# Kernel tuning notes

Hardware: AMD Instinct MI355X
Metric: run time of the kernel (lower is better)

## Reference

```python
import jax, jax.numpy as jnp
import numpy as np

D_MODEL, N_HEADS, D_K, D_V = 1024, 16, 64, 64


def setup_inputs() -> dict:
    key = jax.random.key(0)
    ks = jax.random.split(key, 9)
    B, S = 8, 1024
    Q = jax.random.normal(ks[0], (B, S, D_MODEL), dtype=jnp.float32)
    K = jax.random.normal(ks[1], (B, S, D_MODEL), dtype=jnp.float32)
    V = jax.random.normal(ks[2], (B, S, D_MODEL), dtype=jnp.float32)
    # Xavier-uniform weights (gain=1): limit = sqrt(6/(fan_in+fan_out))
    lim = float(np.sqrt(6.0 / (D_MODEL + N_HEADS * D_K)))
    Wq = jax.random.uniform(ks[3], (D_MODEL, N_HEADS * D_K), minval=-lim, maxval=lim, dtype=jnp.float32)
    Wk = jax.random.uniform(ks[4], (D_MODEL, N_HEADS * D_K), minval=-lim, maxval=lim, dtype=jnp.float32)
    Wv = jax.random.uniform(ks[5], (D_MODEL, N_HEADS * D_V), minval=-lim, maxval=lim, dtype=jnp.float32)
    # nn.Linear default bias init: uniform(-1/sqrt(fan_in), 1/sqrt(fan_in))
    bl = float(1.0 / np.sqrt(D_MODEL))
    bq = jax.random.uniform(ks[6], (N_HEADS * D_K,), minval=-bl, maxval=bl, dtype=jnp.float32)
    bk = jax.random.uniform(ks[7], (N_HEADS * D_K,), minval=-bl, maxval=bl, dtype=jnp.float32)
    bv = jax.random.uniform(ks[8], (N_HEADS * D_V,), minval=-bl, maxval=bl, dtype=jnp.float32)
    return {"Q": Q, "K": K, "V": V, "Wq": Wq, "bq": bq, "Wk": Wk, "bk": bk, "Wv": Wv, "bv": bv}


def reference(Q, K, V, Wq, bq, Wk, bk, Wv, bv):
    B, S, _ = Q.shape
    # projections -> [B, H, S, d]
    q = (Q @ Wq + bq).reshape(B, S, N_HEADS, D_K).transpose(0, 2, 1, 3)
    k = (K @ Wk + bk).reshape(B, S, N_HEADS, D_K).transpose(0, 2, 1, 3)
    v = (V @ Wv + bv).reshape(B, S, N_HEADS, D_V).transpose(0, 2, 1, 3)
    scores = jnp.exp(jnp.einsum('bhqd,bhkd->bhqk', q, k) / jnp.sqrt(jnp.float32(D_K)))
    attn = scores / (jnp.sum(scores, axis=-1, keepdims=True) + 1e-8)
    ctx = jnp.einsum('bhqk,bhkd->bhqd', attn, v)  # [B,H,S,Dv]
    return ctx.transpose(0, 2, 1, 3).reshape(B, S, N_HEADS * D_V)
```

## Files before the change

### kernel.cpp

```cpp
#include <hip/hip_runtime.h>
#include <stdint.h>

#define DM 1024
#define HEADS 16
#define DHEAD 64
#define BATCH 8
#define SEQ 1024
#define MTOT 8192

typedef _Float16 half8 __attribute__((ext_vector_type(8)));
typedef float floatx4 __attribute__((ext_vector_type(4)));

__device__ __forceinline__ void glds16(const void* g, void* l) {
    __builtin_amdgcn_global_load_lds(
        (const __attribute__((address_space(1))) void*)g,
        (__attribute__((address_space(3))) void*)l, 16, 0, 0);
}

__global__ __launch_bounds__(256) void cvt_inputs(
        const float* __restrict__ Q, const float* __restrict__ K,
        const float* __restrict__ V,
        _Float16* __restrict__ qb, _Float16* __restrict__ kb, _Float16* __restrict__ vb) {
    const float* src = blockIdx.y == 0 ? Q : (blockIdx.y == 1 ? K : V);
    _Float16* dst    = blockIdx.y == 0 ? qb : (blockIdx.y == 1 ? kb : vb);
    size_t i = ((size_t)blockIdx.x * 256 + threadIdx.x) * 8;
    float4 a = *(const float4*)(src + i);
    float4 b = *(const float4*)(src + i + 4);
    half8 h;
    h[0] = (_Float16)a.x; h[1] = (_Float16)a.y; h[2] = (_Float16)a.z; h[3] = (_Float16)a.w;
    h[4] = (_Float16)b.x; h[5] = (_Float16)b.y; h[6] = (_Float16)b.z; h[7] = (_Float16)b.w;
    *(half8*)(dst + i) = h;
}

__global__ __launch_bounds__(256) void cvt_w(
        const float* __restrict__ Wq, const float* __restrict__ Wk,
        const float* __restrict__ Wv,
        _Float16* __restrict__ wqt, _Float16* __restrict__ wkt, _Float16* __restrict__ wvt) {
    __shared__ float t[32][33];
    int z = blockIdx.z;
    const float* W = z == 0 ? Wq : (z == 1 ? Wk : Wv);
    _Float16* Wt   = z == 0 ? wqt : (z == 1 ? wkt : wvt);
    int k0 = blockIdx.x * 32, n0 = blockIdx.y * 32;
    int tx = threadIdx.x, ty = threadIdx.y;
#pragma unroll
    for (int i = 0; i < 4; i++)
        t[ty + i * 8][tx] = W[(size_t)(k0 + ty + i * 8) * DM + n0 + tx];
    __syncthreads();
#pragma unroll
    for (int i = 0; i < 4; i++)
        Wt[(size_t)(n0 + ty + i * 8) * DM + k0 + tx] = (_Float16)t[tx][ty + i * 8];
}

__global__ __launch_bounds__(256) void proj_gemm(
        const _Float16* __restrict__ qb, const _Float16* __restrict__ kb,
        const _Float16* __restrict__ vb,
        const _Float16* __restrict__ wqt, const _Float16* __restrict__ wkt,
        const _Float16* __restrict__ wvt,
        const float* __restrict__ bq, const float* __restrict__ bk,
        const float* __restrict__ bv,
        _Float16* __restrict__ qh, _Float16* __restrict__ kh, _Float16* __restrict__ vT) {
    __shared__ _Float16 As[128 * 64];
    __shared__ _Float16 Bs[128 * 64];
    int z = blockIdx.z;
    const _Float16* A  = z == 0 ? qb : (z == 1 ? kb : vb);
    const _Float16* Bw = z == 0 ? wqt : (z == 1 ? wkt : wvt);
    const float* bias  = z == 0 ? bq : (z == 1 ? bk : bv);
    int m0 = blockIdx.x * 128, n0 = blockIdx.y * 128;
    int tid = threadIdx.x, wid = tid >> 6, lane = tid & 63;
    int l15 = lane & 15, quad = lane >> 4;
    int wm = wid >> 1, wn = wid & 1;

    floatx4 acc[4][4] = {};

    for (int kb_ = 0; kb_ < 16; kb_++) {
        __syncthreads();
        int k0 = kb_ * 64;
        int r = (wid * 4) * 8 + (lane >> 3);
        int pg = (lane & 7) ^ (lane >> 3);
#pragma unroll
        for (int ii = 0; ii < 4; ii++) {
            int issue = wid * 4 + ii;
            int rr = r + ii * 8;
            glds16(A  + (size_t)(m0 + rr) * DM + k0 + pg * 8, &As[issue * 512]);
            glds16(Bw + (size_t)(n0 + rr) * DM + k0 + pg * 8, &Bs[issue * 512]);
        }
        __syncthreads();
#pragma unroll
        for (int kc = 0; kc < 2; kc++) {
            half8 a[4], b[4];
#pragma unroll
            for (int mt = 0; mt < 4; mt++) {
                int row = wm * 64 + mt * 16 + l15;
                int pl = (kc * 4 + quad) ^ (l15 & 7);
                a[mt] = *(const half8*)&As[row * 64 + pl * 8];
            }
#pragma unroll
            for (int nt = 0; nt < 4; nt++) {
                int row = wn * 64 + nt * 16 + l15;
                int pl = (kc * 4 + quad) ^ (l15 & 7);
                b[nt] = *(const half8*)&Bs[row * 64 + pl * 8];
            }
#pragma unroll
            for (int mt = 0; mt < 4; mt++)
#pragma unroll
                for (int nt = 0; nt < 4; nt++)
                    acc[mt][nt] = __builtin_amdgcn_mfma_f32_16x16x32_f16(
                        a[mt], b[nt], acc[mt][nt], 0, 0, 0);
        }
    }

    float scale = (z == 0) ? 0.125f : 1.0f;
    _Float16* out = (z == 0) ? qh : ((z == 1) ? kh : vT);
#pragma unroll
    for (int nt = 0; nt < 4; nt++) {
        int col = n0 + wn * 64 + nt * 16 + l15;
        float bv_ = bias[col];
        int h = col >> 6, d = col & 63;
#pragma unroll
        for (int mt = 0; mt < 4; mt++) {
#pragma unroll
            for (int r2 = 0; r2 < 4; r2++) {
                int row = m0 + wm * 64 + mt * 16 + quad * 4 + r2;
                int b_ = row >> 10, s = row & 1023;
                float v = (acc[mt][nt][r2] + bv_) * scale;
                size_t off;
                if (z == 2) off = ((size_t)(b_ * HEADS + h)) * 65536 + (size_t)d * 1024 + s;
                else        off = ((size_t)(b_ * HEADS + h)) * 65536 + (size_t)s * 64 + d;
                out[off] = (_Float16)v;
            }
        }
    }
}

__global__ __launch_bounds__(256) void attn(
        const _Float16* __restrict__ qh, const _Float16* __restrict__ kh,
        const _Float16* __restrict__ vT, float* __restrict__ out) {
    __shared__ _Float16 Qs[4096];
    __shared__ _Float16 Ks[4096];
    __shared__ _Float16 Vs[4096];
    __shared__ _Float16 Ps[4096];
    int qt = blockIdx.x, h = blockIdx.y, b = blockIdx.z;
    size_t base = ((size_t)(b * HEADS + h)) * 65536;
    int tid = threadIdx.x, wid = tid >> 6, lane = tid & 63;
    int l15 = lane & 15, quad = lane >> 4;
    int rs = lane >> 3;
    int pg = (lane & 7) ^ rs;

#pragma unroll
    for (int ii = 0; ii < 2; ii++) {
        int issue = wid * 2 + ii;
        int r = issue * 8 + rs;
        glds16(qh + base + (size_t)(qt * 64 + r) * 64 + pg * 8, &Qs[issue * 512]);
    }
    __syncthreads();
    half8 qf[2];
    {
        int row = wid * 16 + l15;
#pragma unroll
        for (int kc = 0; kc < 2; kc++) {
            int pl = (kc * 4 + quad) ^ (l15 & 7);
            qf[kc] = *(const half8*)&Qs[row * 64 + pl * 8];
        }
    }

    floatx4 oacc[4] = {};
    float rden[4] = {0.f, 0.f, 0.f, 0.f};

    for (int kt = 0; kt < 16; kt++) {
        __syncthreads();
#pragma unroll
        for (int ii = 0; ii < 2; ii++) {
            int issue = wid * 2 + ii;
            int r = issue * 8 + rs;
            glds16(kh + base + (size_t)(kt * 64 + r) * 64 + pg * 8, &Ks[issue * 512]);
            glds16(vT + base + (size_t)r * 1024 + kt * 64 + pg * 8, &Vs[issue * 512]);
        }
        __syncthreads();

        floatx4 sacc[4] = {};
#pragma unroll
        for (int kc = 0; kc < 2; kc++) {
#pragma unroll
            for (int nt = 0; nt < 4; nt++) {
                int row = nt * 16 + l15;
                int pl = (kc * 4 + quad) ^ (l15 & 7);
                half8 bf = *(const half8*)&Ks[row * 64 + pl * 8];
                sacc[nt] = __builtin_amdgcn_mfma_f32_16x16x32_f16(qf[kc], bf, sacc[nt], 0, 0, 0);
            }
        }
#pragma unroll
        for (int nt = 0; nt < 4; nt++) {
            int kj = nt * 16 + l15;
            int pbase = wid * 1024 + (kj >> 3) * 128 + (kj & 7);
#pragma unroll
            for (int j = 0; j < 4; j++) {
                float p = __expf(sacc[nt][j]);
                rden[j] += p;
                Ps[pbase + (quad * 4 + j) * 8] = (_Float16)p;
            }
        }
#pragma unroll
        for (int kc = 0; kc < 2; kc++) {
            half8 af = *(const half8*)&Ps[wid * 1024 + (kc * 4 + quad) * 128 + l15 * 8];
#pragma unroll
            for (int nt = 0; nt < 4; nt++) {
                int row = nt * 16 + l15;
                int pl = (kc * 4 + quad) ^ (l15 & 7);
                half8 bf = *(const half8*)&Vs[row * 64 + pl * 8];
                oacc[nt] = __builtin_amdgcn_mfma_f32_16x16x32_f16(af, bf, oacc[nt], 0, 0, 0);
            }
        }
    }

#pragma unroll
    for (int j = 0; j < 4; j++) {
        float d = rden[j];
        d += __shfl_xor(d, 1, 64);
        d += __shfl_xor(d, 2, 64);
        d += __shfl_xor(d, 4, 64);
        d += __shfl_xor(d, 8, 64);
        rden[j] = 1.0f / (d + 1e-8f);
    }
#pragma unroll
    for (int nt = 0; nt < 4; nt++) {
        int col = h * 64 + nt * 16 + l15;
#pragma unroll
        for (int j = 0; j < 4; j++) {
            int s = qt * 64 + wid * 16 + quad * 4 + j;
            out[((size_t)(b * SEQ + s)) * 1024 + col] = oacc[nt][j] * rden[j];
        }
    }
}

extern "C" void kernel_launch(void* const* d_in, const int* in_sizes, int n_in,
                              void* d_out, int out_size, void* d_ws, size_t ws_size,
                              hipStream_t stream) {
    const float* Q  = (const float*)d_in[0];
    const float* K  = (const float*)d_in[1];
    const float* V  = (const float*)d_in[2];
    const float* Wq = (const float*)d_in[3];
    const float* bq = (const float*)d_in[4];
    const float* Wk = (const float*)d_in[5];
    const float* bk = (const float*)d_in[6];
    const float* Wv = (const float*)d_in[7];
    const float* bv = (const float*)d_in[8];
    float* out = (float*)d_out;

    char* ws = (char*)d_ws;
    const size_t TEN = (size_t)MTOT * DM * sizeof(_Float16);
    _Float16* qb  = (_Float16*)(ws);
    _Float16* kb  = (_Float16*)(ws + TEN);
    _Float16* vb  = (_Float16*)(ws + 2 * TEN);
    _Float16* qh  = (_Float16*)(ws + 3 * TEN);
    _Float16* kh  = (_Float16*)(ws + 4 * TEN);
    _Float16* vT  = (_Float16*)(ws + 5 * TEN);
    const size_t WTN = (size_t)DM * DM * sizeof(_Float16);
    _Float16* wqt = (_Float16*)(ws + 6 * TEN);
    _Float16* wkt = (_Float16*)(ws + 6 * TEN + WTN);
    _Float16* wvt = (_Float16*)(ws + 6 * TEN + 2 * WTN);

    cvt_inputs<<<dim3(4096, 3), 256, 0, stream>>>(Q, K, V, qb, kb, vb);
    cvt_w<<<dim3(32, 32, 3), dim3(32, 8), 0, stream>>>(Wq, Wk, Wv, wqt, wkt, wvt);
    proj_gemm<<<dim3(64, 8, 3), 256, 0, stream>>>(qb, kb, vb, wqt, wkt, wvt,
                                                  bq, bk, bv, qh, kh, vT);
    attn<<<dim3(16, 16, 8), 256, 0, stream>>>(qh, kh, vT, out);
}
```

Baseline: 302.3 us.

## Enlarge attention query tile and vectorize projection epilogue stores via swapped MFMA operands

```diff
diff --git a/kernel.cpp b/kernel.cpp
--- a/kernel.cpp
+++ b/kernel.cpp
@@ -3,12 +3,12 @@
 
 #define DM 1024
 #define HEADS 16
-#define DHEAD 64
 #define BATCH 8
 #define SEQ 1024
 #define MTOT 8192
 
 typedef _Float16 half8 __attribute__((ext_vector_type(8)));
+typedef _Float16 half4 __attribute__((ext_vector_type(4)));
 typedef float floatx4 __attribute__((ext_vector_type(4)));
 
 __device__ __forceinline__ void glds16(const void* g, void* l) {
@@ -69,6 +69,7 @@
     int tid = threadIdx.x, wid = tid >> 6, lane = tid & 63;
     int l15 = lane & 15, quad = lane >> 4;
     int wm = wid >> 1, wn = wid & 1;
+    bool swapped = (z < 2);
 
     floatx4 acc[4][4] = {};
 
@@ -100,33 +101,60 @@
                 int pl = (kc * 4 + quad) ^ (l15 & 7);
                 b[nt] = *(const half8*)&Bs[row * 64 + pl * 8];
             }
-#pragma unroll
-            for (int mt = 0; mt < 4; mt++)
-#pragma unroll
-                for (int nt = 0; nt < 4; nt++)
-                    acc[mt][nt] = __builtin_amdgcn_mfma_f32_16x16x32_f16(
-                        a[mt], b[nt], acc[mt][nt], 0, 0, 0);
-        }
-    }
-
-    float scale = (z == 0) ? 0.125f : 1.0f;
-    _Float16* out = (z == 0) ? qh : ((z == 1) ? kh : vT);
-#pragma unroll
-    for (int nt = 0; nt < 4; nt++) {
-        int col = n0 + wn * 64 + nt * 16 + l15;
-        float bv_ = bias[col];
-        int h = col >> 6, d = col & 63;
-#pragma unroll
-        for (int mt = 0; mt < 4; mt++) {
-#pragma unroll
-            for (int r2 = 0; r2 < 4; r2++) {
-                int row = m0 + wm * 64 + mt * 16 + quad * 4 + r2;
-                int b_ = row >> 10, s = row & 1023;
-                float v = (acc[mt][nt][r2] + bv_) * scale;
-                size_t off;
-                if (z == 2) off = ((size_t)(b_ * HEADS + h)) * 65536 + (size_t)d * 1024 + s;
-                else        off = ((size_t)(b_ * HEADS + h)) * 65536 + (size_t)s * 64 + d;
-                out[off] = (_Float16)v;
+            if (swapped) {
+#pragma unroll
+                for (int mt = 0; mt < 4; mt++)
+#pragma unroll
+                    for (int nt = 0; nt < 4; nt++)
+                        acc[mt][nt] = __builtin_amdgcn_mfma_f32_16x16x32_f16(
+                            b[nt], a[mt], acc[mt][nt], 0, 0, 0);
+            } else {
+#pragma unroll
+                for (int mt = 0; mt < 4; mt++)
+#pragma unroll
+                    for (int nt = 0; nt < 4; nt++)
+                        acc[mt][nt] = __builtin_amdgcn_mfma_f32_16x16x32_f16(
+                            a[mt], b[nt], acc[mt][nt], 0, 0, 0);
+            }
+        }
+    }
+
+    if (swapped) {
+        float sc = (z == 0) ? 0.125f : 1.0f;
+        _Float16* out = (z == 0) ? qh : kh;
+#pragma unroll
+        for (int nt = 0; nt < 4; nt++) {
+            int d0 = n0 + wn * 64 + nt * 16 + quad * 4;
+            int hh = d0 >> 6, dd = d0 & 63;
+            floatx4 b4 = *(const floatx4*)&bias[d0];
+#pragma unroll
+            for (int mt = 0; mt < 4; mt++) {
+                int s = m0 + wm * 64 + mt * 16 + l15;
+                int b_ = s >> 10, ss = s & 1023;
+                size_t off = ((size_t)(b_ * HEADS + hh)) * 65536 + (size_t)ss * 64 + dd;
+                half4 hv;
+#pragma unroll
+                for (int r = 0; r < 4; r++)
+                    hv[r] = (_Float16)((acc[mt][nt][r] + b4[r]) * sc);
+                *(half4*)&out[off] = hv;
+            }
+        }
+    } else {
+#pragma unroll
+        for (int nt = 0; nt < 4; nt++) {
+            int d = n0 + wn * 64 + nt * 16 + l15;
+            int hh = d >> 6, dd = d & 63;
+            float bv_ = bias[d];
+#pragma unroll
+            for (int mt = 0; mt < 4; mt++) {
+                int s0 = m0 + wm * 64 + mt * 16 + quad * 4;
+                int b_ = s0 >> 10, ss = s0 & 1023;
+                size_t off = ((size_t)(b_ * HEADS + hh)) * 65536 + (size_t)dd * 1024 + ss;
+                half4 hv;
+#pragma unroll
+                for (int r = 0; r < 4; r++)
+                    hv[r] = (_Float16)(acc[mt][nt][r] + bv_);
+                *(half4*)&vT[off] = hv;
             }
         }
     }
@@ -135,10 +163,9 @@
 __global__ __launch_bounds__(256) void attn(
         const _Float16* __restrict__ qh, const _Float16* __restrict__ kh,
         const _Float16* __restrict__ vT, float* __restrict__ out) {
-    __shared__ _Float16 Qs[4096];
     __shared__ _Float16 Ks[4096];
     __shared__ _Float16 Vs[4096];
-    __shared__ _Float16 Ps[4096];
+    __shared__ _Float16 QP[16384];
     int qt = blockIdx.x, h = blockIdx.y, b = blockIdx.z;
     size_t base = ((size_t)(b * HEADS + h)) * 65536;
     int tid = threadIdx.x, wid = tid >> 6, lane = tid & 63;
@@ -147,24 +174,26 @@
     int pg = (lane & 7) ^ rs;
 
 #pragma unroll
-    for (int ii = 0; ii < 2; ii++) {
-        int issue = wid * 2 + ii;
+    for (int ii = 0; ii < 8; ii++) {
+        int issue = wid * 8 + ii;
         int r = issue * 8 + rs;
-        glds16(qh + base + (size_t)(qt * 64 + r) * 64 + pg * 8, &Qs[issue * 512]);
+        glds16(qh + base + (size_t)(qt * 256 + r) * 64 + pg * 8, &QP[issue * 512]);
     }
     __syncthreads();
-    half8 qf[2];
-    {
-        int row = wid * 16 + l15;
+    half8 qf[4][2];
+#pragma unroll
+    for (int mt = 0; mt < 4; mt++)
 #pragma unroll
         for (int kc = 0; kc < 2; kc++) {
+            int row = wid * 64 + mt * 16 + l15;
             int pl = (kc * 4 + quad) ^ (l15 & 7);
-            qf[kc] = *(const half8*)&Qs[row * 64 + pl * 8];
-        }
-    }
-
-    floatx4 oacc[4] = {};
+            qf[mt][kc] = *(const half8*)&QP[row * 64 + pl * 8];
+        }
+    __syncthreads();
+
+    floatx4 oacc[4][4] = {};
     float rden[4] = {0.f, 0.f, 0.f, 0.f};
+    _Float16* Pw = &QP[wid * 4096];
 
     for (int kt = 0; kt < 16; kt++) {
         __syncthreads();
@@ -177,57 +206,77 @@
         }
         __syncthreads();
 
-        floatx4 sacc[4] = {};
-#pragma unroll
-        for (int kc = 0; kc < 2; kc++) {
-#pragma unroll
-            for (int nt = 0; nt < 4; nt++) {
-                int row = nt * 16 + l15;
-                int pl = (kc * 4 + quad) ^ (l15 & 7);
-                half8 bf = *(const half8*)&Ks[row * 64 + pl * 8];
-                sacc[nt] = __builtin_amdgcn_mfma_f32_16x16x32_f16(qf[kc], bf, sacc[nt], 0, 0, 0);
-            }
-        }
-#pragma unroll
-        for (int nt = 0; nt < 4; nt++) {
-            int kj = nt * 16 + l15;
-            int pbase = wid * 1024 + (kj >> 3) * 128 + (kj & 7);
-#pragma unroll
-            for (int j = 0; j < 4; j++) {
-                float p = __expf(sacc[nt][j]);
-                rden[j] += p;
-                Ps[pbase + (quad * 4 + j) * 8] = (_Float16)p;
-            }
-        }
-#pragma unroll
-        for (int kc = 0; kc < 2; kc++) {
-            half8 af = *(const half8*)&Ps[wid * 1024 + (kc * 4 + quad) * 128 + l15 * 8];
-#pragma unroll
-            for (int nt = 0; nt < 4; nt++) {
-                int row = nt * 16 + l15;
-                int pl = (kc * 4 + quad) ^ (l15 & 7);
-                half8 bf = *(const half8*)&Vs[row * 64 + pl * 8];
-                oacc[nt] = __builtin_amdgcn_mfma_f32_16x16x32_f16(af, bf, oacc[nt], 0, 0, 0);
-            }
-        }
-    }
-
-#pragma unroll
-    for (int j = 0; j < 4; j++) {
-        float d = rden[j];
-        d += __shfl_xor(d, 1, 64);
-        d += __shfl_xor(d, 2, 64);
-        d += __shfl_xor(d, 4, 64);
-        d += __shfl_xor(d, 8, 64);
-        rden[j] = 1.0f / (d + 1e-8f);
-    }
-#pragma unroll
-    for (int nt = 0; nt < 4; nt++) {
-        int col = h * 64 + nt * 16 + l15;
-#pragma unroll
-        for (int j = 0; j < 4; j++) {
-            int s = qt * 64 + wid * 16 + quad * 4 + j;
-            out[((size_t)(b * SEQ + s)) * 1024 + col] = oacc[nt][j] * rden[j];
+#pragma unroll
+        for (int hf = 0; hf < 2; hf++) {
+            floatx4 sacc[2][4] = {};
+#pragma unroll
+            for (int kc = 0; kc < 2; kc++) {
+                half8 kf[2];
+#pragma unroll
+                for (int kn2 = 0; kn2 < 2; kn2++) {
+                    int kn = hf * 2 + kn2;
+                    int pl = (kc * 4 + quad) ^ (l15 & 7);
+                    kf[kn2] = *(const half8*)&Ks[(kn * 16 + l15) * 64 + pl * 8];
+                }
+#pragma unroll
+                for (int kn2 = 0; kn2 < 2; kn2++)
+#pragma unroll
+                    for (int mt = 0; mt < 4; mt++)
+                        sacc[kn2][mt] = __builtin_amdgcn_mfma_f32_16x16x32_f16(
+                            kf[kn2], qf[mt][kc], sacc[kn2][mt], 0, 0, 0);
+            }
+#pragma unroll
+            for (int kn2 = 0; kn2 < 2; kn2++) {
+                int kn = hf * 2 + kn2;
+#pragma unroll
+                for (int mt = 0; mt < 4; mt++) {
+                    half4 ph;
+#pragma unroll
+                    for (int r = 0; r < 4; r++) {
+                        float p = __expf(sacc[kn2][mt][r]);
+                        rden[mt] += p;
+                        ph[r] = (_Float16)p;
+                    }
+                    *(half4*)&Pw[(kn * 2 + (quad >> 1)) * 512 + (mt * 16 + l15) * 8 +
+                                 (quad & 1) * 4] = ph;
+                }
+            }
+            half8 af[4], vf[4];
+#pragma unroll
+            for (int mt = 0; mt < 4; mt++)
+                af[mt] = *(const half8*)&Pw[(hf * 4 + quad) * 512 + (mt * 16 + l15) * 8];
+#pragma unroll
+            for (int dn = 0; dn < 4; dn++) {
+                int pl = (hf * 4 + quad) ^ (l15 & 7);
+                vf[dn] = *(const half8*)&Vs[(dn * 16 + l15) * 64 + pl * 8];
+            }
+#pragma unroll
+            for (int mt = 0; mt < 4; mt++)
+#pragma unroll
+                for (int dn = 0; dn < 4; dn++)
+                    oacc[mt][dn] = __builtin_amdgcn_mfma_f32_16x16x32_f16(
+                        af[mt], vf[dn], oacc[mt][dn], 0, 0, 0);
+        }
+    }
+
+#pragma unroll
+    for (int mt = 0; mt < 4; mt++) {
+        float d = rden[mt];
+        d += __shfl_xor(d, 16, 64);
+        d += __shfl_xor(d, 32, 64);
+        rden[mt] = 1.0f / (d + 1e-8f);
+    }
+#pragma unroll
+    for (int mt = 0; mt < 4; mt++) {
+#pragma unroll
+        for (int r = 0; r < 4; r++) {
+            float dinv = __shfl(rden[mt], quad * 4 + r, 16);
+            int s = qt * 256 + wid * 64 + mt * 16 + quad * 4 + r;
+#pragma unroll
+            for (int dn = 0; dn < 4; dn++) {
+                int col = h * 64 + dn * 16 + l15;
+                out[((size_t)(b * SEQ + s)) * 1024 + col] = oacc[mt][dn][r] * dinv;
+            }
         }
     }
 }
@@ -263,5 +312,5 @@
     cvt_w<<<dim3(32, 32, 3), dim3(32, 8), 0, stream>>>(Wq, Wk, Wv, wqt, wkt, wvt);
     proj_gemm<<<dim3(64, 8, 3), 256, 0, stream>>>(qb, kb, vb, wqt, wkt, wvt,
                                                   bq, bk, bv, qh, kh, vT);
-    attn<<<dim3(16, 16, 8), 256, 0, stream>>>(qh, kh, vT, out);
-}
+    attn<<<dim3(4, 16, 8), 256, 0, stream>>>(qh, kh, vT, out);
+}
```

Result: faster. 281.3 us, median of 2 (-6.9%).
